# Performance work log

Hardware: AMD Instinct MI355X
Metric: run time of the kernel (lower is better)

## Reference

```python
import jax, jax.numpy as jnp
import numpy as np

SIGMA = 0.2


def setup_inputs() -> dict:
    key = jax.random.key(0)
    k1, k2, k3, k4 = jax.random.split(key, 4)
    n = 50000
    normal = jax.random.normal(k1, (n, 3), dtype=jnp.float32)
    neighbour = jax.random.randint(k2, (n, 3), 0, n, dtype=jnp.int64)
    theta_par = jax.random.uniform(k3, (1, 64, 4), dtype=jnp.float32) * np.pi
    phi_par = jax.random.uniform(k4, (1, 64, 4), dtype=jnp.float32) * (2 * np.pi)
    return {"normal": normal, "neighbour": neighbour,
            "theta_par": theta_par, "phi_par": phi_par}


def reference(normal, neighbour, theta_par, phi_par):
    # kernel points on the unit sphere: [3, 64, 4] (coords, M kernels, L points)
    kernel = jnp.concatenate(
        [jnp.sin(theta_par) * jnp.sin(phi_par),
         jnp.sin(theta_par) * jnp.cos(phi_par),
         jnp.cos(theta_par)], axis=0)
    # gather self + 3 neighbour normals: pts [n, 4, 3]
    neigh = normal[neighbour]                      # [n, 3, 3]
    pts = jnp.concatenate([normal[:, None, :], neigh], axis=1)  # [n, 4, 3]
    # squared distance between each point and each kernel point,
    # summed over coords: [n, 4(points), 64, 4(kernel pts)]
    diff = pts[:, :, :, None, None] - kernel[None, None, :, :, :]
    correl = jnp.sum(diff * diff, axis=2)          # [n, 4, 64, 4]
    resp = jnp.exp(correl / (-2.0 * SIGMA * SIGMA))
    fea = jnp.sum(resp, axis=(1, 3)) / 16.0        # [n, 64]
    return fea
```

## Files before the change

### kernel.cpp

```cpp
#include <hip/hip_runtime.h>
#include <math.h>

#define SIGMA 0.2f
#define LOG2E 1.4426950408889634f

__global__ __launch_bounds__(256) void corr_kernel(
    const float* __restrict__ normal,
    const int*   __restrict__ neighbour,
    const float* __restrict__ theta,
    const float* __restrict__ phi,
    float*       __restrict__ out,
    int n)
{
    __shared__ float kx[256], ky[256], kz[256];
    const int t = threadIdx.x;

    {
        float th = theta[t];
        float ph = phi[t];
        float st = sinf(th), ct = cosf(th);
        float sp = sinf(ph), cp = cosf(ph);
        kx[t] = st * sp;
        ky[t] = st * cp;
        kz[t] = ct;
    }
    __syncthreads();

    const int m = t & 63;
    const int w = t >> 6;

    const float s = LOG2E / (SIGMA * SIGMA);
    float kxs[4], kys[4], kzs[4];
#pragma unroll
    for (int l = 0; l < 4; ++l) {
        kxs[l] = kx[m * 4 + l] * s;
        kys[l] = ky[m * 4 + l] * s;
        kzs[l] = kz[m * 4 + l] * s;
    }
    const float c1 = -LOG2E / (2.0f * SIGMA * SIGMA);

    for (int i = blockIdx.x * 4 + w; i < n; i += gridDim.x * 4) {
        int ids[4];
        ids[0] = i;
        ids[1] = neighbour[i * 3 + 0];
        ids[2] = neighbour[i * 3 + 1];
        ids[3] = neighbour[i * 3 + 2];

        float acc = 0.0f;
#pragma unroll
        for (int p = 0; p < 4; ++p) {
            const float px = normal[ids[p] * 3 + 0];
            const float py = normal[ids[p] * 3 + 1];
            const float pz = normal[ids[p] * 3 + 2];
            const float c2 = (px * px + py * py + pz * pz + 1.0f) * c1;
#pragma unroll
            for (int l = 0; l < 4; ++l) {
                float arg = fmaf(px, kxs[l], fmaf(py, kys[l], fmaf(pz, kzs[l], c2)));
                acc += __builtin_amdgcn_exp2f(arg);
            }
        }
        out[(long long)i * 64 + m] = acc * (1.0f / 16.0f);
    }
}

extern "C" void kernel_launch(void* const* d_in, const int* in_sizes, int n_in,
                              void* d_out, int out_size, void* d_ws, size_t ws_size,
                              hipStream_t stream) {
    const float* normal    = (const float*)d_in[0];
    const int*   neighbour = (const int*)d_in[1];
    const float* theta     = (const float*)d_in[2];
    const float* phi       = (const float*)d_in[3];
    float*       out       = (float*)d_out;

    const int n = in_sizes[0] / 3;

    int blocks = 1024;
    const int max_blocks = (n + 3) / 4;
    if (blocks > max_blocks) blocks = max_blocks;

    hipLaunchKernelGGL(corr_kernel, dim3(blocks), dim3(256), 0, stream,
                       normal, neighbour, theta, phi, out, n);
}
```

Baseline: 20.70 us.

## Replace grid-stride loop with one-point-per-wave 1024-thread blocks and prescaled kernel table

Drops the persistent grid-stride loop. The kernel now launches 1024-thread blocks with one point per wavefront, so each lane handles a single point and all of its gathers are issued up front. The kernel-point table is pre-scaled and stored transposed in shared memory to avoid strided LDS reads, fast __sinf/__cosf intrinsics replace the accurate versions, and the exp2 sum is split into two accumulators to shorten the dependency chain. The cost is that the sincos setup and a block barrier now run once per 16 points instead of being amortized over many, and the fast trig intrinsics lower accuracy slightly.

```diff
diff --git a/kernel.cpp b/kernel.cpp
--- a/kernel.cpp
+++ b/kernel.cpp
@@ -4,7 +4,7 @@
 #define SIGMA 0.2f
 #define LOG2E 1.4426950408889634f
 
-__global__ __launch_bounds__(256) void corr_kernel(
+__global__ __launch_bounds__(1024) void corr_kernel(
     const float* __restrict__ normal,
     const int*   __restrict__ neighbour,
     const float* __restrict__ theta,
@@ -15,52 +15,64 @@
     __shared__ float kx[256], ky[256], kz[256];
     const int t = threadIdx.x;
 
-    {
+    if (t < 256) {
+        const int km = t >> 2;
+        const int kl = t & 3;
         float th = theta[t];
         float ph = phi[t];
-        float st = sinf(th), ct = cosf(th);
-        float sp = sinf(ph), cp = cosf(ph);
-        kx[t] = st * sp;
-        ky[t] = st * cp;
-        kz[t] = ct;
+        float st = __sinf(th), ct = __cosf(th);
+        float sp = __sinf(ph), cp = __cosf(ph);
+        const float s = LOG2E / (SIGMA * SIGMA);
+        kx[kl * 64 + km] = st * sp * s;
+        ky[kl * 64 + km] = st * cp * s;
+        kz[kl * 64 + km] = ct * s;
     }
     __syncthreads();
 
     const int m = t & 63;
     const int w = t >> 6;
+    const int i = blockIdx.x * 16 + w;
+    if (i >= n) return;
 
-    const float s = LOG2E / (SIGMA * SIGMA);
+    const int id1 = neighbour[i * 3 + 0];
+    const int id2 = neighbour[i * 3 + 1];
+    const int id3 = neighbour[i * 3 + 2];
+
+    float px[4], py[4], pz[4];
+    px[0] = normal[(long long)i * 3 + 0];
+    py[0] = normal[(long long)i * 3 + 1];
+    pz[0] = normal[(long long)i * 3 + 2];
+    px[1] = normal[(long long)id1 * 3 + 0];
+    py[1] = normal[(long long)id1 * 3 + 1];
+    pz[1] = normal[(long long)id1 * 3 + 2];
+    px[2] = normal[(long long)id2 * 3 + 0];
+    py[2] = normal[(long long)id2 * 3 + 1];
+    pz[2] = normal[(long long)id2 * 3 + 2];
+    px[3] = normal[(long long)id3 * 3 + 0];
+    py[3] = normal[(long long)id3 * 3 + 1];
+    pz[3] = normal[(long long)id3 * 3 + 2];
+
     float kxs[4], kys[4], kzs[4];
 #pragma unroll
     for (int l = 0; l < 4; ++l) {
-        kxs[l] = kx[m * 4 + l] * s;
-        kys[l] = ky[m * 4 + l] * s;
-        kzs[l] = kz[m * 4 + l] * s;
+        kxs[l] = kx[l * 64 + m];
+        kys[l] = ky[l * 64 + m];
+        kzs[l] = kz[l * 64 + m];
     }
+
     const float c1 = -LOG2E / (2.0f * SIGMA * SIGMA);
 
-    for (int i = blockIdx.x * 4 + w; i < n; i += gridDim.x * 4) {
-        int ids[4];
-        ids[0] = i;
-        ids[1] = neighbour[i * 3 + 0];
-        ids[2] = neighbour[i * 3 + 1];
-        ids[3] = neighbour[i * 3 + 2];
+    float acc0 = 0.0f, acc1 = 0.0f;
+#pragma unroll
+    for (int p = 0; p < 4; ++p) {
+        const float c2 = (px[p] * px[p] + py[p] * py[p] + pz[p] * pz[p] + 1.0f) * c1;
+        acc0 += __builtin_amdgcn_exp2f(fmaf(px[p], kxs[0], fmaf(py[p], kys[0], fmaf(pz[p], kzs[0], c2))));
+        acc1 += __builtin_amdgcn_exp2f(fmaf(px[p], kxs[1], fmaf(py[p], kys[1], fmaf(pz[p], kzs[1], c2))));
+        acc0 += __builtin_amdgcn_exp2f(fmaf(px[p], kxs[2], fmaf(py[p], kys[2], fmaf(pz[p], kzs[2], c2))));
+        acc1 += __builtin_amdgcn_exp2f(fmaf(px[p], kxs[3], fmaf(py[p], kys[3], fmaf(pz[p], kzs[3], c2))));
+    }
 
-        float acc = 0.0f;
-#pragma unroll
-        for (int p = 0; p < 4; ++p) {
-            const float px = normal[ids[p] * 3 + 0];
-            const float py = normal[ids[p] * 3 + 1];
-            const float pz = normal[ids[p] * 3 + 2];
-            const float c2 = (px * px + py * py + pz * pz + 1.0f) * c1;
-#pragma unroll
-            for (int l = 0; l < 4; ++l) {
-                float arg = fmaf(px, kxs[l], fmaf(py, kys[l], fmaf(pz, kzs[l], c2)));
-                acc += __builtin_amdgcn_exp2f(arg);
-            }
-        }
-        out[(long long)i * 64 + m] = acc * (1.0f / 16.0f);
-    }
+    out[(long long)i * 64 + m] = (acc0 + acc1) * (1.0f / 16.0f);
 }
 
 extern "C" void kernel_launch(void* const* d_in, const int* in_sizes, int n_in,
@@ -73,11 +85,8 @@
     float*       out       = (float*)d_out;
 
     const int n = in_sizes[0] / 3;
+    const int blocks = (n + 15) / 16;
 
-    int blocks = 1024;
-    const int max_blocks = (n + 3) / 4;
-    if (blocks > max_blocks) blocks = max_blocks;
-
-    hipLaunchKernelGGL(corr_kernel, dim3(blocks), dim3(256), 0, stream,
+    hipLaunchKernelGGL(corr_kernel, dim3(blocks), dim3(1024), 0, stream,
                        normal, neighbour, theta, phi, out, n);
 }
```

Result: slower. 22.08 us (+6.6%).

## Replace grid-stride loop with one-shot blocks handling two rows per wavefront

Applied to the files above, without the earlier changes.

Drops the persistent grid-stride loop and launches one block per 8 rows, with each wavefront handling two rows whose neighbour and normal gathers are all issued up front. Each thread now computes its own four kernel points from theta/phi with fast sin/cos intrinsics, removing the shared-memory staging and the __syncthreads. Split accumulators add independent exp2 chains for more instruction-level parallelism. The trade-off is redundant trig per thread and a slight accuracy loss from __sinf/__cosf, plus roughly six times as many blocks to launch.

```diff
diff --git a/kernel.cpp b/kernel.cpp
--- a/kernel.cpp
+++ b/kernel.cpp
@@ -4,7 +4,7 @@
 #define SIGMA 0.2f
 #define LOG2E 1.4426950408889634f
 
-__global__ __launch_bounds__(256) void corr_kernel(
+__global__ __launch_bounds__(256) void corr_fused(
     const float* __restrict__ normal,
     const int*   __restrict__ neighbour,
     const float* __restrict__ theta,
@@ -12,55 +12,64 @@
     float*       __restrict__ out,
     int n)
 {
-    __shared__ float kx[256], ky[256], kz[256];
     const int t = threadIdx.x;
-
-    {
-        float th = theta[t];
-        float ph = phi[t];
-        float st = sinf(th), ct = cosf(th);
-        float sp = sinf(ph), cp = cosf(ph);
-        kx[t] = st * sp;
-        ky[t] = st * cp;
-        kz[t] = ct;
-    }
-    __syncthreads();
-
     const int m = t & 63;
     const int w = t >> 6;
+    const int r0 = blockIdx.x * 8 + w * 2;
+    const int r1 = r0 + 1;
+    const int i0 = r0 < n ? r0 : 0;
+    const int i1 = r1 < n ? r1 : 0;
 
+    const int a1 = neighbour[i0 * 3 + 0];
+    const int a2 = neighbour[i0 * 3 + 1];
+    const int a3 = neighbour[i0 * 3 + 2];
+    const int b1 = neighbour[i1 * 3 + 0];
+    const int b2 = neighbour[i1 * 3 + 1];
+    const int b3 = neighbour[i1 * 3 + 2];
+
+    float ax[4], ay[4], az[4], bx[4], by[4], bz[4];
+    ax[0] = normal[i0 * 3 + 0]; ay[0] = normal[i0 * 3 + 1]; az[0] = normal[i0 * 3 + 2];
+    bx[0] = normal[i1 * 3 + 0]; by[0] = normal[i1 * 3 + 1]; bz[0] = normal[i1 * 3 + 2];
+    ax[1] = normal[a1 * 3 + 0]; ay[1] = normal[a1 * 3 + 1]; az[1] = normal[a1 * 3 + 2];
+    ax[2] = normal[a2 * 3 + 0]; ay[2] = normal[a2 * 3 + 1]; az[2] = normal[a2 * 3 + 2];
+    ax[3] = normal[a3 * 3 + 0]; ay[3] = normal[a3 * 3 + 1]; az[3] = normal[a3 * 3 + 2];
+    bx[1] = normal[b1 * 3 + 0]; by[1] = normal[b1 * 3 + 1]; bz[1] = normal[b1 * 3 + 2];
+    bx[2] = normal[b2 * 3 + 0]; by[2] = normal[b2 * 3 + 1]; bz[2] = normal[b2 * 3 + 2];
+    bx[3] = normal[b3 * 3 + 0]; by[3] = normal[b3 * 3 + 1]; bz[3] = normal[b3 * 3 + 2];
+
+    const float4 th = *(const float4*)(theta + 4 * m);
+    const float4 ph = *(const float4*)(phi + 4 * m);
     const float s = LOG2E / (SIGMA * SIGMA);
     float kxs[4], kys[4], kzs[4];
-#pragma unroll
-    for (int l = 0; l < 4; ++l) {
-        kxs[l] = kx[m * 4 + l] * s;
-        kys[l] = ky[m * 4 + l] * s;
-        kzs[l] = kz[m * 4 + l] * s;
+    {
+        const float st0 = __sinf(th.x), st1 = __sinf(th.y), st2 = __sinf(th.z), st3 = __sinf(th.w);
+        const float ct0 = __cosf(th.x), ct1 = __cosf(th.y), ct2 = __cosf(th.z), ct3 = __cosf(th.w);
+        const float sp0 = __sinf(ph.x), sp1 = __sinf(ph.y), sp2 = __sinf(ph.z), sp3 = __sinf(ph.w);
+        const float cp0 = __cosf(ph.x), cp1 = __cosf(ph.y), cp2 = __cosf(ph.z), cp3 = __cosf(ph.w);
+        kxs[0] = st0 * sp0 * s; kys[0] = st0 * cp0 * s; kzs[0] = ct0 * s;
+        kxs[1] = st1 * sp1 * s; kys[1] = st1 * cp1 * s; kzs[1] = ct1 * s;
+        kxs[2] = st2 * sp2 * s; kys[2] = st2 * cp2 * s; kzs[2] = ct2 * s;
+        kxs[3] = st3 * sp3 * s; kys[3] = st3 * cp3 * s; kzs[3] = ct3 * s;
     }
+
     const float c1 = -LOG2E / (2.0f * SIGMA * SIGMA);
 
-    for (int i = blockIdx.x * 4 + w; i < n; i += gridDim.x * 4) {
-        int ids[4];
-        ids[0] = i;
-        ids[1] = neighbour[i * 3 + 0];
-        ids[2] = neighbour[i * 3 + 1];
-        ids[3] = neighbour[i * 3 + 2];
+    float accA0 = 0.0f, accA1 = 0.0f, accB0 = 0.0f, accB1 = 0.0f;
+#pragma unroll
+    for (int p = 0; p < 4; ++p) {
+        const float cA = fmaf(ax[p], ax[p], fmaf(ay[p], ay[p], fmaf(az[p], az[p], 1.0f))) * c1;
+        const float cB = fmaf(bx[p], bx[p], fmaf(by[p], by[p], fmaf(bz[p], bz[p], 1.0f))) * c1;
+#pragma unroll
+        for (int l = 0; l < 4; ++l) {
+            const float gA = fmaf(ax[p], kxs[l], fmaf(ay[p], kys[l], fmaf(az[p], kzs[l], cA)));
+            const float gB = fmaf(bx[p], kxs[l], fmaf(by[p], kys[l], fmaf(bz[p], kzs[l], cB)));
+            if (l & 1) { accA1 += __builtin_amdgcn_exp2f(gA); accB1 += __builtin_amdgcn_exp2f(gB); }
+            else       { accA0 += __builtin_amdgcn_exp2f(gA); accB0 += __builtin_amdgcn_exp2f(gB); }
+        }
+    }
 
-        float acc = 0.0f;
-#pragma unroll
-        for (int p = 0; p < 4; ++p) {
-            const float px = normal[ids[p] * 3 + 0];
-            const float py = normal[ids[p] * 3 + 1];
-            const float pz = normal[ids[p] * 3 + 2];
-            const float c2 = (px * px + py * py + pz * pz + 1.0f) * c1;
-#pragma unroll
-            for (int l = 0; l < 4; ++l) {
-                float arg = fmaf(px, kxs[l], fmaf(py, kys[l], fmaf(pz, kzs[l], c2)));
-                acc += __builtin_amdgcn_exp2f(arg);
-            }
-        }
-        out[(long long)i * 64 + m] = acc * (1.0f / 16.0f);
-    }
+    if (r0 < n) out[r0 * 64 + m] = (accA0 + accA1) * (1.0f / 16.0f);
+    if (r1 < n) out[r1 * 64 + m] = (accB0 + accB1) * (1.0f / 16.0f);
 }
 
 extern "C" void kernel_launch(void* const* d_in, const int* in_sizes, int n_in,
@@ -73,11 +82,8 @@
     float*       out       = (float*)d_out;
 
     const int n = in_sizes[0] / 3;
+    const int blocks = (n + 7) / 8;
 
-    int blocks = 1024;
-    const int max_blocks = (n + 3) / 4;
-    if (blocks > max_blocks) blocks = max_blocks;
-
-    hipLaunchKernelGGL(corr_kernel, dim3(blocks), dim3(256), 0, stream,
+    hipLaunchKernelGGL(corr_fused, dim3(blocks), dim3(256), 0, stream,
                        normal, neighbour, theta, phi, out, n);
 }
```

Result: faster. 19.69 us (-4.9%).
